# Kernel tuning notes

Hardware: AMD Instinct MI355X
Metric: run time of the kernel (lower is better)

## Reference

```python
import jax, jax.numpy as jnp
import numpy as np

B, T, D, H = 4, 2048, 1024, 16
DK = D // H

def setup_inputs() -> dict:
    key = jax.random.key(0)
    ks = jax.random.split(key, 9)
    s = 0.02
    return {
        "x": jax.random.normal(ks[0], (B, T, D), dtype=jnp.float32),
        "Wq": jax.random.normal(ks[1], (D, D), dtype=jnp.float32) * s,
        "bq": jnp.zeros((D,), dtype=jnp.float32),
        "Wk": jax.random.normal(ks[2], (D, D), dtype=jnp.float32) * s,
        "bk": jnp.zeros((D,), dtype=jnp.float32),
        "Wv": jax.random.normal(ks[3], (D, D), dtype=jnp.float32) * s,
        "bv": jnp.zeros((D,), dtype=jnp.float32),
        "Wo": jax.random.normal(ks[4], (D, D), dtype=jnp.float32) * s,
        "bo": jnp.zeros((D,), dtype=jnp.float32),
    }

def reference(x, Wq, bq, Wk, bk, Wv, bv, Wo, bo):
    b, t, c = x.shape
    # projections -> [B, H, T, DK]
    def split_heads(y):
        return y.reshape(b, t, H, DK).transpose(0, 2, 1, 3)
    q = split_heads(x @ Wq.T + bq)
    k = split_heads(x @ Wk.T + bk)
    v = split_heads(x @ Wv.T + bv)
    scale = 1.0 / jnp.sqrt(jnp.asarray(DK, dtype=x.dtype))
    scores = jnp.einsum("bhqd,bhkd->bhqk", q, k) * scale  # [B,H,T,T]
    causal = jnp.tril(jnp.ones((t, t), dtype=bool))
    scores = jnp.where(causal, scores, jnp.asarray(-jnp.inf, dtype=scores.dtype))
    attn = jax.nn.softmax(scores, axis=-1)
    out = jnp.einsum("bhqk,bhkd->bhqd", attn, v)  # [B,H,T,DK]
    out = out.transpose(0, 2, 1, 3).reshape(b, t, c)
    return out @ Wo.T + bo
```

## Files before the change

### kernel.cpp

```cpp
#include <hip/hip_runtime.h>
#include <hip/hip_bf16.h>

#define DEV __device__ __forceinline__

typedef unsigned short u16;
typedef unsigned int u32;
typedef __attribute__((ext_vector_type(4))) float f32x4;
typedef __attribute__((ext_vector_type(16))) float f32x16;
typedef __attribute__((ext_vector_type(8))) __bf16 bf16x8;
typedef __attribute__((ext_vector_type(8))) u16 u16x8;
typedef __attribute__((ext_vector_type(4))) u16 u16x4;
typedef __attribute__((ext_vector_type(4))) u32 u32x4;

#define CSCALE 0.18033688011112042f

DEV u16 f2bf(float f) {
    u32 u = __builtin_bit_cast(u32, f);
    u32 r = (u + 0x7fffu + ((u >> 16) & 1u)) >> 16;
    return (u16)r;
}

DEV u16 f2bf_fast(float f) {
    u32 u = __builtin_bit_cast(u32, f);
    return (u16)((u + 0x8000u) >> 16);
}

DEV float fastrcp(float x) {
#if __has_builtin(__builtin_amdgcn_rcpf)
    return __builtin_amdgcn_rcpf(x);
#else
    return 1.0f / x;
#endif
}

DEV u32 cvtpk_bf16(float lo, float hi) {
    u32 r;
    asm("v_cvt_pk_bf16_f32 %0, %1, %2" : "=v"(r) : "v"(lo), "v"(hi));
    return r;
}

DEV void plswap(u32& a, u32& b) {
    asm volatile("v_permlane32_swap_b32 %0, %1" : "+v"(a), "+v"(b));
}

DEV void gload_lds16(const void* g, void* l) {
    void* gg = const_cast<void*>(g);
    __builtin_amdgcn_global_load_lds(
        (const __attribute__((address_space(1))) void*)gg,
        (__attribute__((address_space(3))) void*)l,
        16, 0, 0);
}

DEV f32x16 mfma32(bf16x8 a, bf16x8 b, f32x16 c) {
    return __builtin_amdgcn_mfma_f32_32x32x16_bf16(a, b, c, 0, 0, 0);
}

__global__ void cvt_f32_bf16(const float* __restrict__ in, u16* __restrict__ out,
                             int n4, float scale) {
    int i = blockIdx.x * blockDim.x + threadIdx.x;
    if (i < n4) {
        float4 v = ((const float4*)in)[i];
        u16x4 o;
        o[0] = f2bf(v.x * scale); o[1] = f2bf(v.y * scale);
        o[2] = f2bf(v.z * scale); o[3] = f2bf(v.w * scale);
        ((u16x4*)out)[i] = o;
    }
}

__global__ void build_bias(const float* __restrict__ bq, const float* __restrict__ bk,
                           const float* __restrict__ bv, float* __restrict__ o) {
    int i = blockIdx.x * blockDim.x + threadIdx.x;
    if (i < 3072) {
        float v;
        if (i < 1024) v = bq[i] * CSCALE;
        else if (i < 2048) v = bk[i - 1024];
        else v = bv[i - 2048];
        o[i] = v;
    }
}

template<int F32OUT>
__global__ __launch_bounds__(256) void gemm_bt(
    const u16* __restrict__ A, const u16* __restrict__ B,
    const float* __restrict__ bias, void* __restrict__ Cv,
    int K, int ldc, int bnPerXcd)
{
    __shared__ u16 As[128 * 64];
    __shared__ u16 Bs[128 * 64];
    const int t = threadIdx.x;
    const int lane = t & 63;
    const int w = t >> 6;
    const int wm = w >> 1, wn = w & 1;
    const int id = (int)blockIdx.x;
    const int xcd = id & 7, r = id >> 3;
    const int bm = (r / bnPerXcd) * 128;
    const int bn = (xcd * bnPerXcd + r % bnPerXcd) * 128;
    const int lr = lane & 15;
    const int lg = lane >> 4;

    f32x4 acc[4][4] = {};

    for (int k0 = 0; k0 < K; k0 += 64) {
        #pragma unroll
        for (int i = 0; i < 4; ++i) {
            int off = (t + i * 256) * 16;
            int row = off >> 7;
            int colb = off & 127;
            gload_lds16((const char*)A + ((size_t)(bm + row) * K + k0) * 2 + colb,
                        (char*)As + off);
            gload_lds16((const char*)B + ((size_t)(bn + row) * K + k0) * 2 + colb,
                        (char*)Bs + off);
        }
        __syncthreads();
        #pragma unroll
        for (int kk = 0; kk < 2; ++kk) {
            bf16x8 af[4], bfr[4];
            #pragma unroll
            for (int m = 0; m < 4; ++m)
                af[m] = *(const bf16x8*)&As[(wm * 64 + m * 16 + lr) * 64 + kk * 32 + lg * 8];
            #pragma unroll
            for (int n = 0; n < 4; ++n)
                bfr[n] = *(const bf16x8*)&Bs[(wn * 64 + n * 16 + lr) * 64 + kk * 32 + lg * 8];
            #pragma unroll
            for (int m = 0; m < 4; ++m)
                #pragma unroll
                for (int n = 0; n < 4; ++n)
                    acc[m][n] = __builtin_amdgcn_mfma_f32_16x16x32_bf16(af[m], bfr[n], acc[m][n], 0, 0, 0);
        }
        __syncthreads();
    }

    #pragma unroll
    for (int n = 0; n < 4; ++n) {
        int col = bn + wn * 64 + n * 16 + lr;
        float bv = bias[col];
        #pragma unroll
        for (int m = 0; m < 4; ++m) {
            int row0 = bm + wm * 64 + m * 16 + lg * 4;
            #pragma unroll
            for (int r2 = 0; r2 < 4; ++r2) {
                float v = acc[m][n][r2] + bv;
                size_t idx = (size_t)(row0 + r2) * ldc + col;
                if (F32OUT) ((float*)Cv)[idx] = v;
                else        ((u16*)Cv)[idx] = f2bf(v);
            }
        }
    }
}

__global__ __launch_bounds__(256, 2) void attn_fwd(
    const u16* __restrict__ QKV, u16* __restrict__ Om)
{
    constexpr int T = 2048, LD = 3072, DO = 1024;
    constexpr int PSTR = 72;
    constexpr float NEG = -3.0e38f;

    __shared__ __align__(16) u16 Ks[2][64 * 64];
    __shared__ __align__(16) u16 Vt[2][64 * PSTR];

    const int t = threadIdx.x, lane = t & 63, w = t >> 6;
    const int ql = lane & 31, hi = lane >> 5;

    const int id = (int)blockIdx.x;
    const int slot = id >> 6;
    const int bh = (id & 7) * 8 + ((id >> 3) & 7);
    const int q0 = (15 - slot) * 128;
    const int b = bh >> 4, h = bh & 15;
    const size_t rowbase = (size_t)b * T * LD + h * 64;
    const u16* Qm = QKV + rowbase;
    const u16* Km = QKV + rowbase + 1024;
    const u16* Vm = QKV + rowbase + 2048;
    const int nt = q0 / 64 + 2;

    const int qg = q0 + w * 32 + ql;
    const int qmax = q0 + w * 32 + 31;

    bf16x8 qf[4];
    {
        const u16* qp = Qm + (size_t)qg * LD + hi * 8;
        #pragma unroll
        for (int s = 0; s < 4; ++s) qf[s] = *(const bf16x8*)(qp + s * 16);
    }

    f32x16 oa[2] = {};
    float lsum = 0.f;

    const int krow = t >> 3, kslot = t & 7;
    const u16* kCur = Km + (size_t)krow * LD + 8 * (kslot ^ (krow & 7));
    const int kv2 = (t & 31) * 2, dd = (t >> 5) * 8;
    const u16* vCur = Vm + (size_t)kv2 * LD + dd;
    u16x8 vva, vvb;

    auto stageK = [&](int buf) {
        u16* dst = (u16*)Ks + buf * 4096 + t * 8;
        gload_lds16(kCur, dst);
        gload_lds16(kCur + 32 * LD, dst + 2048);
        kCur += 64 * LD;
    };
    auto loadV = [&]() {
        vva = *(const u16x8*)vCur;
        vvb = *(const u16x8*)(vCur + LD);
        vCur += 64 * LD;
    };
    auto writeVt = [&](int buf) {
        u32* vd = (u32*)((u16*)Vt + buf * (64 * PSTR) + dd * PSTR + kv2);
        #pragma unroll
        for (int j = 0; j < 8; ++j)
            vd[j * (PSTR / 2)] = (u32)vva[j] | ((u32)vvb[j] << 16);
    };

    stageK(0);
    loadV();
    writeVt(0);

    for (int it0 = 0; it0 < nt; it0 += 2) {
        #pragma unroll
        for (int half = 0; half < 2; ++half) {
            const int BUF = half;
            const int it = it0 + half;
            const int kv0 = it * 64;
            __syncthreads();

            const bool more = (it + 1 < nt);
            if (more) { stageK(BUF ^ 1); loadV(); }

            const bool a0  = kv0 <= qmax;
            const bool a0h = kv0 + 32 <= qmax;

            f32x16 sa[2] = {};
            __builtin_amdgcn_s_setprio(1);
            #pragma unroll
            for (int n = 0; n < 2; ++n) {
                if (!(n ? a0h : a0)) continue;
                const int row = n * 32 + ql;
                const int swz = (row & 7) << 4;
                #pragma unroll
                for (int s = 0; s < 4; ++s) {
                    bf16x8 kf = *(const bf16x8*)((const char*)Ks + BUF * 8192 + row * 128 +
                                                 ((((s << 1) | hi) << 4) ^ swz));
                    sa[n] = mfma32(kf, qf[s], sa[n]);
                }
            }
            __builtin_amdgcn_s_setprio(0);

            u32x4 pw[2][2];
            if (a0) {
                float rs = 0.f;
                #pragma unroll
                for (int n = 0; n < 2; ++n) {
                    if (n == 1 && !a0h) continue;
                    if (kv0 + n * 32 + 31 > q0 + w * 32) {
                        #pragma unroll
                        for (int r = 0; r < 16; ++r) {
                            int kvg = kv0 + n * 32 + (r & 3) + 8 * (r >> 2) + 4 * hi;
                            if (kvg > qg) sa[n][r] = NEG;
                        }
                    }
                    float pv[16];
                    #pragma unroll
                    for (int r = 0; r < 16; ++r)
                        pv[r] = __builtin_exp2f(sa[n][r]);
                    float s8[8];
                    #pragma unroll
                    for (int r = 0; r < 8; ++r) s8[r] = pv[r] + pv[r + 8];
                    rs += ((s8[0] + s8[4]) + (s8[1] + s8[5])) + ((s8[2] + s8[6]) + (s8[3] + s8[7]));
                    #pragma unroll
                    for (int s = 0; s < 2; ++s) {
                        u32 u0 = cvtpk_bf16(pv[8 * s + 0], pv[8 * s + 1]);
                        u32 u1 = cvtpk_bf16(pv[8 * s + 2], pv[8 * s + 3]);
                        u32 u2 = cvtpk_bf16(pv[8 * s + 4], pv[8 * s + 5]);
                        u32 u3 = cvtpk_bf16(pv[8 * s + 6], pv[8 * s + 7]);
                        plswap(u0, u2);
                        plswap(u1, u3);
                        pw[n][s] = u32x4{u0, u1, u2, u3};
                    }
                }
                rs += __shfl_xor(rs, 32);
                lsum += rs;
            }

            __builtin_amdgcn_s_setprio(1);
            #pragma unroll
            for (int dt = 0; dt < 2; ++dt) {
                const int vrow = dt * 32 + ql;
                #pragma unroll
                for (int n = 0; n < 2; ++n) {
                    if (!(n ? a0h : a0)) continue;
                    #pragma unroll
                    for (int s = 0; s < 2; ++s) {
                        bf16x8 vf = *(const bf16x8*)((const u16*)Vt + BUF * (64 * PSTR) +
                                                     vrow * PSTR + n * 32 + s * 16 + hi * 8);
                        oa[dt] = mfma32(vf, __builtin_bit_cast(bf16x8, pw[n][s]), oa[dt]);
                    }
                }
            }
            __builtin_amdgcn_s_setprio(0);

            if (more) writeVt(BUF ^ 1);
        }
    }

    __syncthreads();
    u16* ot = ((u16*)Vt) + w * (32 * PSTR);
    const float inv = fastrcp(lsum);
    #pragma unroll
    for (int dt = 0; dt < 2; ++dt)
        #pragma unroll
        for (int r = 0; r < 16; ++r) {
            int d = dt * 32 + (r & 3) + 8 * (r >> 2) + 4 * hi;
            ot[ql * PSTR + d] = f2bf_fast(oa[dt][r] * inv);
        }
    const int lq = lane >> 1, hv = lane & 1;
    const size_t obase = (size_t)b * T * DO + h * 64;
    const u16* src = ot + lq * PSTR + hv * 32;
    u16* dst = Om + obase + (size_t)(q0 + w * 32 + lq) * DO + hv * 32;
    #pragma unroll
    for (int seg = 0; seg < 4; ++seg)
        *(u16x8*)(dst + seg * 8) = *(const u16x8*)(src + seg * 8);
}

extern "C" void kernel_launch(void* const* d_in, const int* in_sizes, int n_in,
                              void* d_out, int out_size, void* d_ws, size_t ws_size,
                              hipStream_t stream)
{
    const float* x  = (const float*)d_in[0];
    const float* Wq = (const float*)d_in[1];
    const float* bq = (const float*)d_in[2];
    const float* Wk = (const float*)d_in[3];
    const float* bk = (const float*)d_in[4];
    const float* Wv = (const float*)d_in[5];
    const float* bv = (const float*)d_in[6];
    const float* Wo = (const float*)d_in[7];
    const float* bo = (const float*)d_in[8];

    constexpr int T = 2048, D = 1024;
    constexpr size_t MT = (size_t)4 * T;

    const size_t NEED = (size_t)74 << 20;
    if (ws_size < NEED) return;

    char* ws = (char*)d_ws;
    u16* xb    = (u16*)(ws);
    u16* Ob    = (u16*)(ws);
    u16* Wqkvb = (u16*)(ws + ((size_t)16 << 20));
    u16* Wob   = (u16*)(ws + ((size_t)22 << 20));
    u16* QKVb  = (u16*)(ws + ((size_t)24 << 20));
    float* bqkv = (float*)(ws + ((size_t)72 << 20));

    int nx4 = (int)(MT * D / 4);
    cvt_f32_bf16<<<(nx4 + 255) / 256, 256, 0, stream>>>(x, xb, nx4, 1.0f);
    int nw4 = D * D / 4;
    cvt_f32_bf16<<<(nw4 + 255) / 256, 256, 0, stream>>>(Wq, Wqkvb, nw4, CSCALE);
    cvt_f32_bf16<<<(nw4 + 255) / 256, 256, 0, stream>>>(Wk, Wqkvb + (size_t)D * D, nw4, 1.0f);
    cvt_f32_bf16<<<(nw4 + 255) / 256, 256, 0, stream>>>(Wv, Wqkvb + (size_t)2 * D * D, nw4, 1.0f);
    cvt_f32_bf16<<<(nw4 + 255) / 256, 256, 0, stream>>>(Wo, Wob, nw4, 1.0f);
    build_bias<<<12, 256, 0, stream>>>(bq, bk, bv, bqkv);

    gemm_bt<0><<<dim3(1536), 256, 0, stream>>>(xb, Wqkvb, bqkv, QKVb, D, 3072, 3);

    attn_fwd<<<dim3(1024), 256, 0, stream>>>(QKVb, Ob);

    gemm_bt<1><<<dim3(512), 256, 0, stream>>>(Ob, Wob, bo, d_out, D, 1024, 1);
}
```

Measured before the change: 189.2 us.

## Rewrite projection GEMMs with larger tiles, LDS double buffering, swizzle, staged stores

Replaces the 128x128 single-buffered GEMM with 512-thread blocks computing 256xBN tiles. K-tiles are double-buffered in LDS so the next tile's global loads overlap MFMA work, using explicit vmcnt waits. LDS reads use an XOR swizzle to avoid bank conflicts, and MFMA sections get raised priority. The bf16 output is staged through LDS for coalesced 16-byte stores. Larger tiles cut global traffic per FLOP, but the grid is smaller (384 and 256 blocks) and the XCD-aware block mapping is dropped, which may hurt occupancy and L2 locality.

```diff
diff --git a/kernel.cpp b/kernel.cpp
--- a/kernel.cpp
+++ b/kernel.cpp
@@ -79,70 +79,146 @@
     }
 }
 
-template<int F32OUT>
-__global__ __launch_bounds__(256) void gemm_bt(
+template<int NFRAG, int F32OUT>
+__global__ __launch_bounds__(512, 2) void gemm_bt2(
     const u16* __restrict__ A, const u16* __restrict__ B,
     const float* __restrict__ bias, void* __restrict__ Cv,
-    int K, int ldc, int bnPerXcd)
+    int K, int ldc, int ncols)
 {
-    __shared__ u16 As[128 * 64];
-    __shared__ u16 Bs[128 * 64];
+    constexpr int BN = NFRAG * 64;
+    constexpr int ABUF = 256 * 64;
+    constexpr int BBUF = BN * 64;
+    __shared__ __align__(16) u16 lds[2 * ABUF + 2 * BBUF];
+    u16* As = lds;
+    u16* Bs = lds + 2 * ABUF;
+
     const int t = threadIdx.x;
-    const int lane = t & 63;
-    const int w = t >> 6;
-    const int wm = w >> 1, wn = w & 1;
+    const int lane = t & 63, w = t >> 6;
+    const int wm = w >> 2, wn = w & 3;
+    const int lr = lane & 15, lg = lane >> 4;
+    const int swz = (lr & 7) << 4;
+
     const int id = (int)blockIdx.x;
-    const int xcd = id & 7, r = id >> 3;
-    const int bm = (r / bnPerXcd) * 128;
-    const int bn = (xcd * bnPerXcd + r % bnPerXcd) * 128;
-    const int lr = lane & 15;
-    const int lg = lane >> 4;
-
-    f32x4 acc[4][4] = {};
-
-    for (int k0 = 0; k0 < K; k0 += 64) {
+    const int bm = (id / ncols) * 256;
+    const int bn = (id % ncols) * BN;
+    const int NT = K >> 6;
+
+    const u16* aSrc[4];
+    const u16* bSrc[NFRAG];
+    #pragma unroll
+    for (int i = 0; i < 4; ++i) {
+        int idx = t + i * 512, row = idx >> 3, g = idx & 7;
+        aSrc[i] = A + (size_t)(bm + row) * K + (g ^ (row & 7)) * 8;
+    }
+    #pragma unroll
+    for (int i = 0; i < NFRAG; ++i) {
+        int idx = t + i * 512, row = idx >> 3, g = idx & 7;
+        bSrc[i] = B + (size_t)(bn + row) * K + (g ^ (row & 7)) * 8;
+    }
+
+    auto stage = [&](int buf) {
         #pragma unroll
         for (int i = 0; i < 4; ++i) {
-            int off = (t + i * 256) * 16;
-            int row = off >> 7;
-            int colb = off & 127;
-            gload_lds16((const char*)A + ((size_t)(bm + row) * K + k0) * 2 + colb,
-                        (char*)As + off);
-            gload_lds16((const char*)B + ((size_t)(bn + row) * K + k0) * 2 + colb,
-                        (char*)Bs + off);
-        }
-        __syncthreads();
-        #pragma unroll
-        for (int kk = 0; kk < 2; ++kk) {
-            bf16x8 af[4], bfr[4];
-            #pragma unroll
-            for (int m = 0; m < 4; ++m)
-                af[m] = *(const bf16x8*)&As[(wm * 64 + m * 16 + lr) * 64 + kk * 32 + lg * 8];
-            #pragma unroll
-            for (int n = 0; n < 4; ++n)
-                bfr[n] = *(const bf16x8*)&Bs[(wn * 64 + n * 16 + lr) * 64 + kk * 32 + lg * 8];
-            #pragma unroll
-            for (int m = 0; m < 4; ++m)
-                #pragma unroll
-                for (int n = 0; n < 4; ++n)
-                    acc[m][n] = __builtin_amdgcn_mfma_f32_16x16x32_bf16(af[m], bfr[n], acc[m][n], 0, 0, 0);
-        }
-        __syncthreads();
-    }
-
-    #pragma unroll
-    for (int n = 0; n < 4; ++n) {
-        int col = bn + wn * 64 + n * 16 + lr;
-        float bv = bias[col];
-        #pragma unroll
-        for (int m = 0; m < 4; ++m) {
-            int row0 = bm + wm * 64 + m * 16 + lg * 4;
-            #pragma unroll
-            for (int r2 = 0; r2 < 4; ++r2) {
-                float v = acc[m][n][r2] + bv;
-                size_t idx = (size_t)(row0 + r2) * ldc + col;
-                if (F32OUT) ((float*)Cv)[idx] = v;
-                else        ((u16*)Cv)[idx] = f2bf(v);
+            gload_lds16(aSrc[i], As + buf * ABUF + (t + i * 512) * 8);
+            aSrc[i] += 64;
+        }
+        #pragma unroll
+        for (int i = 0; i < NFRAG; ++i) {
+            gload_lds16(bSrc[i], Bs + buf * BBUF + (t + i * 512) * 8);
+            bSrc[i] += 64;
+        }
+    };
+    auto wait_lps = [&]() {
+        if constexpr (NFRAG == 4) asm volatile("s_waitcnt vmcnt(8)" ::: "memory");
+        else                      asm volatile("s_waitcnt vmcnt(6)" ::: "memory");
+    };
+
+    f32x4 acc[8][NFRAG] = {};
+
+    stage(0); stage(1);
+    wait_lps();
+    __builtin_amdgcn_s_barrier();
+
+    for (int kt0 = 0; kt0 < NT; kt0 += 2) {
+        #pragma unroll
+        for (int hh = 0; hh < 2; ++hh) {
+            const int BUF = hh;
+            const int kt = kt0 + hh;
+
+            #pragma unroll
+            for (int kk = 0; kk < 2; ++kk) {
+                bf16x8 af[8], bfr[NFRAG];
+                #pragma unroll
+                for (int m = 0; m < 8; ++m)
+                    af[m] = *(const bf16x8*)((const char*)As + BUF * (ABUF * 2) +
+                             (wm * 128 + m * 16 + lr) * 128 + ((kk * 64 + lg * 16) ^ swz));
+                #pragma unroll
+                for (int n = 0; n < NFRAG; ++n)
+                    bfr[n] = *(const bf16x8*)((const char*)Bs + BUF * (BBUF * 2) +
+                              (wn * (NFRAG * 16) + n * 16 + lr) * 128 + ((kk * 64 + lg * 16) ^ swz));
+                __builtin_amdgcn_s_setprio(1);
+                #pragma unroll
+                for (int m = 0; m < 8; ++m)
+                    #pragma unroll
+                    for (int n = 0; n < NFRAG; ++n)
+                        acc[m][n] = __builtin_amdgcn_mfma_f32_16x16x32_bf16(af[m], bfr[n], acc[m][n], 0, 0, 0);
+                __builtin_amdgcn_s_setprio(0);
+            }
+
+            asm volatile("s_waitcnt lgkmcnt(0)" ::: "memory");
+            __builtin_amdgcn_s_barrier();
+            if (kt + 2 < NT) {
+                stage(BUF);
+                wait_lps();
+            } else {
+                asm volatile("s_waitcnt vmcnt(0)" ::: "memory");
+            }
+            __builtin_amdgcn_s_barrier();
+        }
+    }
+
+    const int wcol = bn + wn * (NFRAG * 16);
+    if constexpr (F32OUT) {
+        #pragma unroll
+        for (int n = 0; n < NFRAG; ++n) {
+            int col = wcol + n * 16 + lr;
+            float bvv = bias[col];
+            #pragma unroll
+            for (int m = 0; m < 8; ++m) {
+                int row0 = bm + wm * 128 + m * 16 + lg * 4;
+                #pragma unroll
+                for (int r = 0; r < 4; ++r)
+                    ((float*)Cv)[(size_t)(row0 + r) * ldc + col] = acc[m][n][r] + bvv;
+            }
+        }
+    } else {
+        float bv[NFRAG];
+        #pragma unroll
+        for (int n = 0; n < NFRAG; ++n) bv[n] = bias[wcol + n * 16 + lr];
+        u16* ot = lds + w * (64 * 72);
+        const int rowR = lane >> 1, segC = (lane & 1) * 32;
+        #pragma unroll
+        for (int pass = 0; pass < 2; ++pass) {
+            if (pass) asm volatile("s_waitcnt lgkmcnt(0)" ::: "memory");
+            #pragma unroll
+            for (int mm = 0; mm < 4; ++mm) {
+                #pragma unroll
+                for (int n = 0; n < NFRAG; ++n)
+                    #pragma unroll
+                    for (int r = 0; r < 4; ++r)
+                        ot[(mm * 16 + lg * 4 + r) * 72 + n * 16 + lr] =
+                            f2bf(acc[pass * 4 + mm][n][r] + bv[n]);
+            }
+            asm volatile("s_waitcnt lgkmcnt(0)" ::: "memory");
+            #pragma unroll
+            for (int half = 0; half < 2; ++half) {
+                int row_l = rowR + half * 32;
+                int grow = bm + wm * 128 + pass * 64 + row_l;
+                const u16* src = ot + row_l * 72 + segC;
+                u16* dst = (u16*)Cv + (size_t)grow * ldc + wcol + segC;
+                #pragma unroll
+                for (int s2 = 0; s2 < 4; ++s2)
+                    *(u16x8*)(dst + s2 * 8) = *(const u16x8*)(src + s2 * 8);
             }
         }
     }
@@ -356,9 +432,9 @@
     cvt_f32_bf16<<<(nw4 + 255) / 256, 256, 0, stream>>>(Wo, Wob, nw4, 1.0f);
     build_bias<<<12, 256, 0, stream>>>(bq, bk, bv, bqkv);
 
-    gemm_bt<0><<<dim3(1536), 256, 0, stream>>>(xb, Wqkvb, bqkv, QKVb, D, 3072, 3);
+    gemm_bt2<4, 0><<<dim3(384), 512, 0, stream>>>(xb, Wqkvb, bqkv, QKVb, D, 3072, 12);
 
     attn_fwd<<<dim3(1024), 256, 0, stream>>>(QKVb, Ob);
 
-    gemm_bt<1><<<dim3(512), 256, 0, stream>>>(Ob, Wob, bo, d_out, D, 1024, 1);
-}
+    gemm_bt2<2, 1><<<dim3(256), 512, 0, stream>>>(Ob, Wob, bo, d_out, D, 1024, 8);
+}
```

After: 186.9 us. About the same (-1.2%).
